# Optimization experiments

Hardware: AMD Instinct MI355X
Metric: run time of the kernel (lower is better)

The kernel has to match this reference:

```python
import jax, jax.numpy as jnp
import numpy as np

S, IN_DIM = 16384, 1024
NUM_PROJ, PROJ_DIM, BINS = 100, 64, 20
D = NUM_PROJ * PROJ_DIM
EPS = 1e-12  # F.normalize eps


def setup_inputs() -> dict:
    key = jax.random.key(0)
    kx, kw = jax.random.split(key)
    x = jax.random.normal(kx, (S, IN_DIM), dtype=jnp.float32)
    W = jax.random.normal(kw, (D, IN_DIM), dtype=jnp.float32)  # nn.Linear weight, std=1.0 init
    # mins/maxs as produced by cal_min_max over the data (per projected dim)
    proj = x @ W.T
    mins = jnp.min(proj, axis=0)
    maxs = jnp.max(proj, axis=0)
    return {"x": x, "W": W, "mins": mins, "maxs": maxs,
            "num_of_projection": NUM_PROJ, "bins": BINS}


def reference(x, W, mins, maxs, num_of_projection, bins):
    # get_global_feature(x, normalize=True), all histograms fused via scatter-add
    proj = x @ W.T                                   # [S, D]
    d = proj.shape[1]
    proj_dim = d // num_of_projection
    width = maxs - mins                              # [D]
    # torch.histc semantics: values in [min, max] counted; value == max -> last bin
    idx = jnp.floor((proj - mins) / width * bins).astype(jnp.int32)
    idx = jnp.clip(idx, 0, bins - 1)
    valid = (proj >= mins) & (proj <= maxs)
    flat = idx + jnp.arange(d, dtype=jnp.int32)[None, :] * bins   # [S, D]
    hist = jnp.zeros(d * bins, dtype=proj.dtype).at[flat.reshape(-1)].add(
        valid.reshape(-1).astype(proj.dtype))
    gv = hist.reshape(num_of_projection, proj_dim, bins)
    # F.normalize(p=2, dim=2)
    norm = jnp.linalg.norm(gv, axis=2, keepdims=True)
    gv = gv / jnp.maximum(norm, EPS)
    return gv
```

## Files before the change

### kernel.cpp

```cpp
#include <hip/hip_runtime.h>
#include <cmath>

#define S_DIM 16384
#define K_DIM 1024
#define D_DIM 6400
#define NBINS 20
#define HSTRIDE 21

using half_t = _Float16;
using half8  = __attribute__((ext_vector_type(8))) _Float16;
using f32x4  = __attribute__((ext_vector_type(4))) float;

__global__ void cvt_f32_f16(const float* __restrict__ a, half_t* __restrict__ da, int n8a,
                            const float* __restrict__ b, half_t* __restrict__ db, int n8b,
                            float4* __restrict__ z, int nz4) {
  int i = blockIdx.x * blockDim.x + threadIdx.x;
  if (i < nz4) z[i] = (float4){0.f, 0.f, 0.f, 0.f};
  const float* s; half_t* d; int idx;
  if (i < n8a) { s = a; d = da; idx = i; }
  else { idx = i - n8a; if (idx >= n8b) return; s = b; d = db; }
  float4 v0 = ((const float4*)s)[idx * 2];
  float4 v1 = ((const float4*)s)[idx * 2 + 1];
  half8 h = { (half_t)v0.x, (half_t)v0.y, (half_t)v0.z, (half_t)v0.w,
              (half_t)v1.x, (half_t)v1.y, (half_t)v1.z, (half_t)v1.w };
  ((half8*)d)[idx] = h;
}

#define VMWAIT0() __asm__ volatile("s_waitcnt vmcnt(0)" ::: "memory")
#define BAR()     __asm__ volatile("s_barrier" ::: "memory")
#define SP1()     __builtin_amdgcn_s_setprio(1)
#define SP0()     __builtin_amdgcn_s_setprio(0)

#define GLL(SRC, DST) __builtin_amdgcn_global_load_lds(                      \
    (const __attribute__((address_space(1))) void*)(SRC),                    \
    (__attribute__((address_space(3))) void*)(DST), 16, 0, 0)

__global__ __launch_bounds__(1024, 4) void gemm_hist256(
    const half_t* __restrict__ xh, const half_t* __restrict__ wh,
    const float* __restrict__ mins, const float* __restrict__ maxs,
    int* __restrict__ ghist)
{
  __shared__ __align__(16) char ldsA[2 * 32768];
  __shared__ __align__(16) char ldsB[2 * 32768];
  __shared__ int shist[256 * HSTRIDE];

  const int t    = threadIdx.x;
  const int lane = t & 63;
  const int wv   = t >> 6;
  const int wm   = wv >> 2;
  const int wn   = wv & 3;
  const int l16  = lane & 15;
  const int quad = lane >> 4;

  const int bid = blockIdx.x;
  const int wg  = (bid & 7) * 200 + (bid >> 3);
  const int ct  = wg / 64;
  const int rt  = wg - ct * 64;
  const int colBase = ct * 256;
  const int rowBase = rt * 256;

  for (int i = t; i < 256 * HSTRIDE; i += 1024) shist[i] = 0;

  const char* pA0 = ldsA + (wm * 64 + l16) * 128 + (((0 + quad) ^ (l16 & 7)) * 16);
  const char* pA1 = ldsA + (wm * 64 + l16) * 128 + (((4 + quad) ^ (l16 & 7)) * 16);
  const char* pB0 = ldsB + (wn * 64 + l16) * 128 + (((0 + quad) ^ (l16 & 7)) * 16);
  const char* pB1 = ldsB + (wn * 64 + l16) * 128 + (((4 + quad) ^ (l16 & 7)) * 16);

  const int gOff = (t >> 3) * K_DIM + (((t & 7) ^ ((t >> 3) & 7)) * 8);
  const int wvD  = wv * 1024;

  const half_t* xS = xh + (size_t)rowBase * K_DIM + gOff;
  const half_t* wS = wh + (size_t)colBase * K_DIM + gOff;

  f32x4 acc[4][4];
#pragma unroll
  for (int m = 0; m < 4; ++m)
#pragma unroll
    for (int n = 0; n < 4; ++n) acc[m][n] = (f32x4){0.f, 0.f, 0.f, 0.f};

  half8 aF[4], bF[4];

#define MFMA16()                                                             \
  _Pragma("unroll") for (int mf = 0; mf < 4; ++mf)                           \
  _Pragma("unroll") for (int nf = 0; nf < 4; ++nf)                           \
    acc[mf][nf] = __builtin_amdgcn_mfma_f32_16x16x32_f16(                    \
        aF[mf], bF[nf], acc[mf][nf], 0, 0, 0);

  GLL(xS,          ldsA + wvD);
  GLL(xS + 131072, ldsA + 16384 + wvD);
  GLL(wS,          ldsB + wvD);
  GLL(wS + 131072, ldsB + 16384 + wvD);
  VMWAIT0(); BAR();

  const half_t* xStg = xS + 64;
  const half_t* wStg = wS + 64;

#define TILE(PB, PN, STG)                                                    \
  {                                                                          \
    if (STG) {                                                               \
      GLL(xStg,          ldsA + (PN) + wvD);                                 \
      GLL(xStg + 131072, ldsA + (PN) + 16384 + wvD);                         \
      GLL(wStg,          ldsB + (PN) + wvD);                                 \
      GLL(wStg + 131072, ldsB + (PN) + 16384 + wvD);                         \
      xStg += 64; wStg += 64;                                                \
    }                                                                        \
    _Pragma("unroll") for (int mf = 0; mf < 4; ++mf)                         \
      aF[mf] = *(const half8*)(pA0 + (PB) + mf * 2048);                      \
    _Pragma("unroll") for (int nf = 0; nf < 4; ++nf)                         \
      bF[nf] = *(const half8*)(pB0 + (PB) + nf * 2048);                      \
    SP1(); MFMA16(); SP0();                                                  \
    _Pragma("unroll") for (int mf = 0; mf < 4; ++mf)                         \
      aF[mf] = *(const half8*)(pA1 + (PB) + mf * 2048);                      \
    _Pragma("unroll") for (int nf = 0; nf < 4; ++nf)                         \
      bF[nf] = *(const half8*)(pB1 + (PB) + nf * 2048);                      \
    SP1(); MFMA16(); SP0();                                                  \
    VMWAIT0(); BAR();                                                        \
  }

#pragma unroll 1
  for (int it = 0; it < 7; ++it) {
    TILE(0,     32768, 1);
    TILE(32768, 0,     1);
  }
  TILE(0,     32768, 1);
  TILE(32768, 0,     0);

#undef TILE

#pragma unroll
  for (int nf = 0; nf < 4; ++nf) {
    const int lc = wn * 64 + nf * 16 + l16;
    const float a = mins[colBase + lc], b = maxs[colBase + lc];
    const float sc = (float)NBINS / (b - a);
    int* colHist = &shist[lc * HSTRIDE];
#pragma unroll
    for (int mf = 0; mf < 4; ++mf) {
#pragma unroll
      for (int r = 0; r < 4; ++r) {
        float v = acc[mf][nf][r];
        if (v >= a && v <= b) {
          int bin = (int)((v - a) * sc);
          bin = bin > NBINS - 1 ? NBINS - 1 : bin;
          atomicAdd(&colHist[bin], 1);
        }
      }
    }
  }
  __syncthreads();
  for (int i = t; i < 256 * NBINS; i += 1024) {
    int col = i / NBINS, bin = i - col * NBINS;
    int v = shist[col * HSTRIDE + bin];
    if (v) atomicAdd(&ghist[colBase * NBINS + i], v);
  }
}

__global__ __launch_bounds__(256) void gemm_hist_fb(
    const float* __restrict__ xf, const float* __restrict__ wf,
    const float* __restrict__ mins, const float* __restrict__ maxs,
    int* __restrict__ ghist)
{
  __shared__ __align__(16) half_t ldsA[4096];
  __shared__ __align__(16) half_t ldsB[4096];
  __shared__ int shist[128 * HSTRIDE];

  const int t     = threadIdx.x;
  const int lane  = t & 63;
  const int wv    = t >> 6;
  const int waveM = wv >> 1;
  const int waveN = wv & 1;
  const int l16   = lane & 15;
  const int quad  = lane >> 4;
  const int colBase = blockIdx.x * 128;

  for (int i = t; i < 128 * HSTRIDE; i += 256) shist[i] = 0;

  float mn[4], mx[4], inv[4];
  int lcol[4];
#pragma unroll
  for (int nt = 0; nt < 4; ++nt) {
    int lc = waveN * 64 + nt * 16 + l16;
    lcol[nt] = lc;
    float a = mins[colBase + lc], b = maxs[colBase + lc];
    mn[nt] = a; mx[nt] = b;
    inv[nt] = (float)NBINS / (b - a);
  }

  int aOff[4], bOff[4];
#pragma unroll
  for (int mt = 0; mt < 4; ++mt) {
    int m = waveM * 64 + mt * 16 + l16;
    aOff[mt] = (m * 4 + (quad ^ ((m >> 1) & 3))) * 8;
  }
#pragma unroll
  for (int nt = 0; nt < 4; ++nt) {
    int n = waveN * 64 + nt * 16 + l16;
    bOff[nt] = (n * 4 + (quad ^ ((n >> 1) & 3))) * 8;
  }

  for (int rt = blockIdx.y; rt < S_DIM / 128; rt += gridDim.y) {
    const int rowBase = rt * 128;
    f32x4 acc[4][4];
#pragma unroll
    for (int mt = 0; mt < 4; ++mt)
#pragma unroll
      for (int nt = 0; nt < 4; ++nt) acc[mt][nt] = (f32x4){0.f, 0.f, 0.f, 0.f};

    for (int kt = 0; kt < K_DIM; kt += 32) {
      __syncthreads();
#pragma unroll
      for (int i = 0; i < 2; ++i) {
        const int seg = t + i * 256;
        const int row = seg >> 2;
        const int kch = (seg & 3) ^ ((row >> 1) & 3);
        const float* ga = xf + (size_t)(rowBase + row) * K_DIM + kt + kch * 8;
        float4 v0 = ((const float4*)ga)[0];
        float4 v1 = ((const float4*)ga)[1];
        half8 h = { (half_t)v0.x, (half_t)v0.y, (half_t)v0.z, (half_t)v0.w,
                    (half_t)v1.x, (half_t)v1.y, (half_t)v1.z, (half_t)v1.w };
        *(half8*)&ldsA[seg * 8] = h;
        const float* gb = wf + (size_t)(colBase + row) * K_DIM + kt + kch * 8;
        float4 u0 = ((const float4*)gb)[0];
        float4 u1 = ((const float4*)gb)[1];
        half8 g = { (half_t)u0.x, (half_t)u0.y, (half_t)u0.z, (half_t)u0.w,
                    (half_t)u1.x, (half_t)u1.y, (half_t)u1.z, (half_t)u1.w };
        *(half8*)&ldsB[seg * 8] = g;
      }
      __syncthreads();
      {
        half8 aFf[4], bFf[4];
#pragma unroll
        for (int mt = 0; mt < 4; ++mt) aFf[mt] = *(const half8*)&ldsA[aOff[mt]];
#pragma unroll
        for (int nt = 0; nt < 4; ++nt) bFf[nt] = *(const half8*)&ldsB[bOff[nt]];
#pragma unroll
        for (int mt = 0; mt < 4; ++mt)
#pragma unroll
          for (int nt = 0; nt < 4; ++nt)
            acc[mt][nt] = __builtin_amdgcn_mfma_f32_16x16x32_f16(
                aFf[mt], bFf[nt], acc[mt][nt], 0, 0, 0);
      }
    }

#pragma unroll
    for (int nt = 0; nt < 4; ++nt) {
      const float a = mn[nt], b = mx[nt], sc = inv[nt];
      int* colHist = &shist[lcol[nt] * HSTRIDE];
#pragma unroll
      for (int mt = 0; mt < 4; ++mt) {
#pragma unroll
        for (int r = 0; r < 4; ++r) {
          float v = acc[mt][nt][r];
          if (v >= a && v <= b) {
            int bin = (int)((v - a) * sc);
            bin = bin > NBINS - 1 ? NBINS - 1 : bin;
            atomicAdd(&colHist[bin], 1);
          }
        }
      }
    }
  }

  __syncthreads();
  for (int i = t; i < 128 * NBINS; i += 256) {
    int col = i / NBINS, bin = i - col * NBINS;
    int v = shist[col * HSTRIDE + bin];
    if (v) atomicAdd(&ghist[colBase * NBINS + i], v);
  }
}

__global__ void normalize_kernel(const int* __restrict__ hist, float* __restrict__ out) {
  int g = blockIdx.x * blockDim.x + threadIdx.x;
  if (g >= D_DIM) return;
  const int base = g * NBINS;
  float v[NBINS];
  float ss = 0.f;
#pragma unroll
  for (int i = 0; i < NBINS; ++i) { v[i] = (float)hist[base + i]; ss += v[i] * v[i]; }
  float sc = 1.0f / fmaxf(sqrtf(ss), 1e-12f);
#pragma unroll
  for (int i = 0; i < NBINS; ++i) out[base + i] = v[i] * sc;
}

extern "C" void kernel_launch(void* const* d_in, const int* in_sizes, int n_in,
                              void* d_out, int out_size, void* d_ws, size_t ws_size,
                              hipStream_t stream) {
  const float* x    = (const float*)d_in[0];
  const float* W    = (const float*)d_in[1];
  const float* mins = (const float*)d_in[2];
  const float* maxs = (const float*)d_in[3];
  float* out = (float*)d_out;

  const size_t xh_elems = (size_t)S_DIM * K_DIM;
  const size_t wh_elems = (size_t)D_DIM * K_DIM;
  const size_t need = (xh_elems + wh_elems) * sizeof(half_t);

  if (ws_size >= need) {
    half_t* xh = (half_t*)d_ws;
    half_t* wh = xh + xh_elems;
    int n8x = (int)(xh_elems / 8), n8w = (int)(wh_elems / 8);
    int tot = n8x + n8w;
    cvt_f32_f16<<<(tot + 255) / 256, 256, 0, stream>>>(
        x, xh, n8x, W, wh, n8w, (float4*)d_out, out_size / 4);
    gemm_hist256<<<dim3(1600), 1024, 0, stream>>>(xh, wh, mins, maxs, (int*)d_out);
  } else {
    hipMemsetAsync(d_out, 0, (size_t)out_size * sizeof(float), stream);
    gemm_hist_fb<<<dim3(D_DIM / 128, 64), 256, 0, stream>>>(
        x, W, mins, maxs, (int*)d_out);
  }

  normalize_kernel<<<(D_DIM + 255) / 256, 256, 0, stream>>>((int*)d_out, out);
}
```

Before: 366.6 us.

## Shrink GEMM-histogram tile to 128x256 with 512 threads and K-step 32

Replaces the 256x256 block tile (1024 threads, K-step 64) with a 128x256 tile (512 threads, K-step 32), doubling the grid to 3200 blocks. LDS staging shrinks to 16 KB for A and 32 KB for B across the two buffers, and the swizzle is rewritten for 64-byte rows. The aim is a smaller LDS footprint so more blocks fit per CU, which should raise occupancy and overlap. The cost is less data reuse per block, twice as many barriers per K, and twice as many per-block histogram flushes to global memory.

```diff
diff --git a/kernel.cpp b/kernel.cpp
--- a/kernel.cpp
+++ b/kernel.cpp
@@ -35,13 +35,13 @@
     (const __attribute__((address_space(1))) void*)(SRC),                    \
     (__attribute__((address_space(3))) void*)(DST), 16, 0, 0)
 
-__global__ __launch_bounds__(1024, 4) void gemm_hist256(
+__global__ __launch_bounds__(512, 4) void gemm_hist128(
     const half_t* __restrict__ xh, const half_t* __restrict__ wh,
     const float* __restrict__ mins, const float* __restrict__ maxs,
     int* __restrict__ ghist)
 {
-  __shared__ __align__(16) char ldsA[2 * 32768];
-  __shared__ __align__(16) char ldsB[2 * 32768];
+  __shared__ __align__(16) char ldsA[2 * 8192];
+  __shared__ __align__(16) char ldsB[2 * 16384];
   __shared__ int shist[256 * HSTRIDE];
 
   const int t    = threadIdx.x;
@@ -53,20 +53,19 @@
   const int quad = lane >> 4;
 
   const int bid = blockIdx.x;
-  const int wg  = (bid & 7) * 200 + (bid >> 3);
-  const int ct  = wg / 64;
-  const int rt  = wg - ct * 64;
+  const int wg  = (bid & 7) * 400 + (bid >> 3);
+  const int ct  = wg / 128;
+  const int rt  = wg - ct * 128;
   const int colBase = ct * 256;
-  const int rowBase = rt * 256;
-
-  for (int i = t; i < 256 * HSTRIDE; i += 1024) shist[i] = 0;
-
-  const char* pA0 = ldsA + (wm * 64 + l16) * 128 + (((0 + quad) ^ (l16 & 7)) * 16);
-  const char* pA1 = ldsA + (wm * 64 + l16) * 128 + (((4 + quad) ^ (l16 & 7)) * 16);
-  const char* pB0 = ldsB + (wn * 64 + l16) * 128 + (((0 + quad) ^ (l16 & 7)) * 16);
-  const char* pB1 = ldsB + (wn * 64 + l16) * 128 + (((4 + quad) ^ (l16 & 7)) * 16);
-
-  const int gOff = (t >> 3) * K_DIM + (((t & 7) ^ ((t >> 3) & 7)) * 8);
+  const int rowBase = rt * 128;
+
+  for (int i = t; i < 256 * HSTRIDE; i += 512) shist[i] = 0;
+
+  const int swz = (quad ^ ((l16 >> 1) & 3)) * 16;
+  const char* pA = ldsA + (wm * 64 + l16) * 64 + swz;
+  const char* pB = ldsB + (wn * 64 + l16) * 64 + swz;
+
+  const int gOff = (t >> 2) * K_DIM + (((t & 3) ^ ((t >> 3) & 3)) * 8);
   const int wvD  = wv * 1024;
 
   const half_t* xS = xh + (size_t)rowBase * K_DIM + gOff;
@@ -86,44 +85,37 @@
     acc[mf][nf] = __builtin_amdgcn_mfma_f32_16x16x32_f16(                    \
         aF[mf], bF[nf], acc[mf][nf], 0, 0, 0);
 
-  GLL(xS,          ldsA + wvD);
-  GLL(xS + 131072, ldsA + 16384 + wvD);
-  GLL(wS,          ldsB + wvD);
-  GLL(wS + 131072, ldsB + 16384 + wvD);
+  GLL(xS,                ldsA + wvD);
+  GLL(wS,                ldsB + wvD);
+  GLL(wS + 128 * K_DIM,  ldsB + 8192 + wvD);
   VMWAIT0(); BAR();
 
-  const half_t* xStg = xS + 64;
-  const half_t* wStg = wS + 64;
-
-#define TILE(PB, PN, STG)                                                    \
+  const half_t* xStg = xS + 32;
+  const half_t* wStg = wS + 32;
+
+#define TILE(PA, PBb, NA, NBb, STG)                                          \
   {                                                                          \
     if (STG) {                                                               \
-      GLL(xStg,          ldsA + (PN) + wvD);                                 \
-      GLL(xStg + 131072, ldsA + (PN) + 16384 + wvD);                         \
-      GLL(wStg,          ldsB + (PN) + wvD);                                 \
-      GLL(wStg + 131072, ldsB + (PN) + 16384 + wvD);                         \
-      xStg += 64; wStg += 64;                                                \
+      GLL(xStg,               ldsA + (NA) + wvD);                            \
+      GLL(wStg,               ldsB + (NBb) + wvD);                           \
+      GLL(wStg + 128 * K_DIM, ldsB + (NBb) + 8192 + wvD);                    \
+      xStg += 32; wStg += 32;                                                \
     }                                                                        \
     _Pragma("unroll") for (int mf = 0; mf < 4; ++mf)                         \
-      aF[mf] = *(const half8*)(pA0 + (PB) + mf * 2048);                      \
+      aF[mf] = *(const half8*)(pA + (PA) + mf * 1024);                       \
     _Pragma("unroll") for (int nf = 0; nf < 4; ++nf)                         \
-      bF[nf] = *(const half8*)(pB0 + (PB) + nf * 2048);                      \
-    SP1(); MFMA16(); SP0();                                                  \
-    _Pragma("unroll") for (int mf = 0; mf < 4; ++mf)                         \
-      aF[mf] = *(const half8*)(pA1 + (PB) + mf * 2048);                      \
-    _Pragma("unroll") for (int nf = 0; nf < 4; ++nf)                         \
-      bF[nf] = *(const half8*)(pB1 + (PB) + nf * 2048);                      \
+      bF[nf] = *(const half8*)(pB + (PBb) + nf * 1024);                      \
     SP1(); MFMA16(); SP0();                                                  \
     VMWAIT0(); BAR();                                                        \
   }
 
 #pragma unroll 1
-  for (int it = 0; it < 7; ++it) {
-    TILE(0,     32768, 1);
-    TILE(32768, 0,     1);
-  }
-  TILE(0,     32768, 1);
-  TILE(32768, 0,     0);
+  for (int it = 0; it < 15; ++it) {
+    TILE(0,    0,     8192, 16384, 1);
+    TILE(8192, 16384, 0,    0,     1);
+  }
+  TILE(0,    0,     8192, 16384, 1);
+  TILE(8192, 16384, 0,    0,     0);
 
 #undef TILE
 
@@ -147,7 +139,7 @@
     }
   }
   __syncthreads();
-  for (int i = t; i < 256 * NBINS; i += 1024) {
+  for (int i = t; i < 256 * NBINS; i += 512) {
     int col = i / NBINS, bin = i - col * NBINS;
     int v = shist[col * HSTRIDE + bin];
     if (v) atomicAdd(&ghist[colBase * NBINS + i], v);
@@ -301,7 +293,7 @@
     int tot = n8x + n8w;
     cvt_f32_f16<<<(tot + 255) / 256, 256, 0, stream>>>(
         x, xh, n8x, W, wh, n8w, (float4*)d_out, out_size / 4);
-    gemm_hist256<<<dim3(1600), 1024, 0, stream>>>(xh, wh, mins, maxs, (int*)d_out);
+    gemm_hist128<<<dim3(3200), 512, 0, stream>>>(xh, wh, mins, maxs, (int*)d_out);
   } else {
     hipMemsetAsync(d_out, 0, (size_t)out_size * sizeof(float), stream);
     gemm_hist_fb<<<dim3(D_DIM / 128, 64), 256, 0, stream>>>(
```

Measured after the change: 401.3 us. +9.5%, slower.
